# Kernel optimization log

Hardware: AMD Instinct MI355X
Metric: run time of the kernel (lower is better)

Reference implementation:

```python
import jax, jax.numpy as jnp
import numpy as np

ALPHA = 0.2
NEG_INF = -9e15


def setup_inputs() -> dict:
    key = jax.random.key(0)
    k1, k2, k3, k4 = jax.random.split(key, 4)
    B, N, C_IN, C_OUT, R, H = 8, 1024, 256, 256, 4, 4
    node_feats = jax.random.normal(k1, (B, N, C_IN), dtype=jnp.float32)
    adj_matrix = jax.random.randint(k2, (B, N, N, R), 0, 2, dtype=jnp.int32)
    # xavier_uniform with gain=1.414 for Linear(c_in, c_out) weights
    lim_w = 1.414 * np.sqrt(6.0 / (C_IN + C_OUT))
    W = jax.random.uniform(k3, (R, C_IN, C_OUT), minval=-lim_w, maxval=lim_w, dtype=jnp.float32)
    c_per = C_OUT // H
    lim_a = 1.414 * np.sqrt(6.0 / (H + 2 * c_per))
    a = jax.random.uniform(k4, (R, H, 2 * c_per), minval=-lim_a, maxval=lim_a, dtype=jnp.float32)
    return {"node_feats": node_feats, "adj_matrix": adj_matrix, "W": W, "a": a}


def reference(node_feats, adj_matrix, W, a):
    B, N, _ = node_feats.shape
    R, H = a.shape[0], a.shape[1]
    C = a.shape[2] // 2  # per-head feature dim
    out = jnp.zeros((B, N, H, C), dtype=node_feats.dtype)
    for r in range(R):
        # per-relation projection: [B,N,H,C]
        f = jnp.einsum('bnc,cd->bnd', node_feats, W[r]).reshape(B, N, H, C)
        a_l, a_r = a[r, :, :C], a[r, :, C:]
        # attention logit decomposes: a . [f_i || f_j] = a_l . f_i + a_r . f_j
        li = jnp.einsum('bnhc,hc->bnh', f, a_l)  # source-node term
        lj = jnp.einsum('bnhc,hc->bnh', f, a_r)  # target-node term
        logits = jax.nn.leaky_relu(li[:, :, None, :] + lj[:, None, :, :], ALPHA)  # [B,N,N,H]
        mask = adj_matrix[..., r] != 0  # [B,N,N]
        logits = jnp.where(mask[..., None], logits, NEG_INF)
        probs = jax.nn.softmax(logits, axis=2)
        out = out + jnp.einsum('bijh,bjhc->bihc', probs, f)
    # concat_heads=True
    return out.reshape(B, N, H * C)
```

## Files before the change

kernel.cpp:

```cpp
#include <hip/hip_runtime.h>
#include <math.h>

#define Bsz 8
#define Nn 1024
#define CIN 256
#define COUT 256
#define NR 4
#define NH 4

typedef unsigned short u16;
typedef __attribute__((ext_vector_type(8))) short bf16x8;
typedef __attribute__((ext_vector_type(4))) float f32x4;
typedef __attribute__((ext_vector_type(2))) float f32x2;

#define OFF_LIP (16u << 20)
#define OFF_LJP ((16u << 20) + (512u << 10))
#define OFF_ADJM (17u << 20)
#define OFF_XBF (21u << 20)
#define OFF_WFRAG (25u << 20)
#define OFF_WAL ((25u << 20) + (512u << 10))
#define OFF_WAR ((25u << 20) + (528u << 10))

#define LOG2E 1.4426950408889634f

__device__ __forceinline__ short f2bf(float x) {
  union { float f; unsigned u; } v; v.f = x;
  unsigned r = (v.u + 0x7FFFu + ((v.u >> 16) & 1u)) >> 16;
  return (short)r;
}

__device__ __forceinline__ float fast_exp2(float x) {
#if __has_builtin(__builtin_amdgcn_exp2f)
  return __builtin_amdgcn_exp2f(x);
#else
  return exp2f(x);
#endif
}

__device__ __forceinline__ int sbfe1(unsigned v, int bit) {
#if __has_builtin(__builtin_amdgcn_sbfe)
  return __builtin_amdgcn_sbfe((int)v, bit, 1);
#else
  return ((int)(v << (31 - bit))) >> 31;
#endif
}

__device__ __forceinline__ unsigned perm_hi16(unsigned hi, unsigned lo) {
#if __has_builtin(__builtin_amdgcn_perm)
  return __builtin_amdgcn_perm(hi, lo, 0x07060302u);
#else
  return (lo >> 16) | (hi & 0xFFFF0000u);
#endif
}

__global__ __launch_bounds__(256, 4)
void gatt_packprep(const int4* __restrict__ adj4, const float* __restrict__ W,
                   const float* __restrict__ a, unsigned long long* __restrict__ adjm,
                   u16* __restrict__ Wfrag, float* __restrict__ wa_l,
                   float* __restrict__ wa_r) {
  const int t = threadIdx.x;
  if (blockIdx.x < 32768) {
    const int wid = blockIdx.x * 4 + (t >> 6);
    const int lane = t & 63;
    const int jw = wid & 15;
    const int i = (wid >> 4) & 1023;
    const int b = wid >> 14;
    const int j = jw * 64 + lane;
    const int4 av = adj4[(size_t)(b * Nn + i) * Nn + j];
    const unsigned long long b0 = __ballot(av.x != 0);
    const unsigned long long b1 = __ballot(av.y != 0);
    const unsigned long long b2 = __ballot(av.z != 0);
    const unsigned long long b3 = __ballot(av.w != 0);
    if (lane < 4) {
      unsigned long long v = (lane == 0) ? b0 : (lane == 1) ? b1 : (lane == 2) ? b2 : b3;
      adjm[((size_t)((b * Nn + i) * NR + lane)) * 16 + jw] = v;
    }
  } else if (blockIdx.x < 32768 + 32) {
    const int bid2 = blockIdx.x - 32768;
    const int r = bid2 >> 3, kc = bid2 & 7;
    const int cg = t >> 4, mm = t & 15;
    float wv[32];
#pragma unroll 8
    for (int kk = 0; kk < 32; ++kk)
      wv[kk] = W[(size_t)r * 65536 + (size_t)(kc * 32 + kk) * COUT + t];
    u16* base = Wfrag + (size_t)r * 65536 + (size_t)(cg * 8 + kc) * 512 + mm * 8;
#pragma unroll
    for (int quad = 0; quad < 4; ++quad) {
      u16 pk[8];
#pragma unroll
      for (int e = 0; e < 8; ++e) pk[e] = (u16)f2bf(wv[quad * 8 + e]);
      *(int4*)(base + quad * 128) = *(int4*)pk;
    }
  } else {
    const int cb = blockIdx.x - 32768 - 32;
    const int r = cb >> 2, h = cb & 3;
    float sl = 0.f, sr = 0.f;
    const float* Wp = W + (size_t)r * 65536 + (size_t)t * COUT + h * 64;
    const float* ap = a + r * 512 + h * 128;
#pragma unroll 8
    for (int c = 0; c < 64; ++c) {
      const float wv = Wp[c];
      sl = fmaf(wv, ap[c], sl);
      sr = fmaf(wv, ap[64 + c], sr);
    }
    wa_l[(size_t)cb * CIN + t] = sl;
    wa_r[(size_t)cb * CIN + t] = sr;
  }
}

__global__ __launch_bounds__(256, 4)
void gatt_logitx(const float* __restrict__ X, const float4* __restrict__ wal4,
                 const float4* __restrict__ war4, float* __restrict__ Lip,
                 float* __restrict__ Ljp, u16* __restrict__ Xbf) {
  __shared__ float Xs[16 * 260];
  const int t = threadIdx.x;
  const int row0 = blockIdx.x * 16;
  {
    const int il = t >> 4, kq = t & 15;
    const float4* xp = (const float4*)(X + (size_t)(row0 + il) * CIN + kq * 16);
    float4 v[4];
    u16 pk[16];
#pragma unroll
    for (int u = 0; u < 4; ++u) {
      v[u] = xp[u];
      pk[u * 4 + 0] = (u16)f2bf(v[u].x);
      pk[u * 4 + 1] = (u16)f2bf(v[u].y);
      pk[u * 4 + 2] = (u16)f2bf(v[u].z);
      pk[u * 4 + 3] = (u16)f2bf(v[u].w);
    }
    float4* dst = (float4*)(Xs + il * 260 + kq * 16);
#pragma unroll
    for (int u = 0; u < 4; ++u) dst[u] = v[u];
    u16* xb = Xbf + (size_t)(row0 + il) * CIN + kq * 16;
    *(int4*)xb = *(int4*)pk;
    *(int4*)(xb + 8) = *(int4*)(pk + 8);
  }
  __syncthreads();
  const int rl = t >> 4, combo = t & 15;
  float li = 0.f, lj = 0.f;
#pragma unroll 8
  for (int k4 = 0; k4 < 64; ++k4) {
    const float4 x4 = *(const float4*)(Xs + rl * 260 + k4 * 4);
    const float4 wl = wal4[combo * 64 + k4];
    const float4 wr = war4[combo * 64 + k4];
    li += x4.x * wl.x + x4.y * wl.y + x4.z * wl.z + x4.w * wl.w;
    lj += x4.x * wr.x + x4.y * wr.y + x4.z * wr.z + x4.w * wr.w;
  }
  const int g = row0 + rl, b = g >> 10, n = g & 1023;
  const size_t idx = ((size_t)(combo * Bsz + b)) * Nn + n;
  Lip[idx] = li * LOG2E;
  Ljp[idx] = lj * LOG2E;
}

__global__ __launch_bounds__(256, 4)
void gatt_fgemm(const u16* __restrict__ Xbf, const u16* __restrict__ Wfrag,
                u16* __restrict__ fTf) {
  const int t = threadIdx.x;
  const int r = blockIdx.x & 3, b = (blockIdx.x >> 2) & 7, ntl = blockIdx.x >> 5;
  const int n0 = ntl * 32;
  const int lane = t & 63, w = t >> 6;
  const int m = lane & 15, quad = lane >> 4;

  const u16* wbase = Wfrag + (size_t)r * 65536 + (size_t)(w * 4) * 8 * 512 + lane * 8;
  const u16* xbase = Xbf + (size_t)(b * Nn + n0 + m) * CIN + quad * 8;

  f32x4 acc[4][2];
#pragma unroll
  for (int ct = 0; ct < 4; ++ct)
#pragma unroll
    for (int nt = 0; nt < 2; ++nt) acc[ct][nt] = (f32x4){0.f, 0.f, 0.f, 0.f};

#pragma unroll
  for (int kc = 0; kc < 8; ++kc) {
    bf16x8 af[4], bfr[2];
#pragma unroll
    for (int ct = 0; ct < 4; ++ct)
      af[ct] = *(const bf16x8*)(wbase + (size_t)(ct * 8 + kc) * 512);
#pragma unroll
    for (int nt = 0; nt < 2; ++nt)
      bfr[nt] = *(const bf16x8*)(xbase + (size_t)(nt * 16) * CIN + kc * 32);
#pragma unroll
    for (int ct = 0; ct < 4; ++ct)
#pragma unroll
      for (int nt = 0; nt < 2; ++nt)
        acc[ct][nt] = __builtin_amdgcn_mfma_f32_16x16x32_bf16(af[ct], bfr[nt], acc[ct][nt], 0, 0, 0);
  }

  u16* fragbase = fTf + (size_t)(((r * Bsz + b) * 4 + w) * 128) * 512;
  const int jb = n0 >> 5;
  const int e = m & 7;
#pragma unroll
  for (int ct = 0; ct < 4; ++ct) {
#pragma unroll
    for (int nt = 0; nt < 2; ++nt) {
      const int qt = nt * 2 + (m >> 3);
      u16* dst = fragbase + (size_t)((jb * 4 + ct) * 512) + (qt * 16 + quad * 4) * 8 + e;
#pragma unroll
      for (int p = 0; p < 4; ++p) dst[p * 8] = (u16)f2bf(acc[ct][nt][p]);
    }
  }
}

__global__ __launch_bounds__(256, 4)
void gatt_attn(const unsigned long long* __restrict__ adjm,
               const u16* __restrict__ fTf, const float* __restrict__ Lip,
               const float* __restrict__ Ljp, float* __restrict__ out) {
  const int t = threadIdx.x;
  const int b = blockIdx.x & 7;
  const int i0 = (blockIdx.x >> 3) * 16;
  const int h = t >> 6, lane = t & 63;
  const int m = lane & 15, quad = lane >> 4;
  const int qo = quad * 8;

  bf16x8 ones;
#pragma unroll
  for (int e = 0; e < 8; ++e) ones[e] = (short)0x3F80;

  float outsum[4][4];
#pragma unroll
  for (int nt = 0; nt < 4; ++nt)
#pragma unroll
    for (int p = 0; p < 4; ++p) outsum[nt][p] = 0.f;

  for (int r = 0; r < NR; ++r) {
    const float liv = Lip[((size_t)((r * NH + h) * Bsz + b)) * Nn + i0 + m];
    const float* ljh = Ljp + ((size_t)((r * NH + h) * Bsz + b)) * Nn;
    const unsigned long long* amp = adjm + ((size_t)((b * Nn + i0 + m) * NR + r)) * 16;
    const bf16x8* fp = (const bf16x8*)fTf + (size_t)((r * Bsz + b) * 4 + h) * 8192;

    f32x4 acc[4], den;
    den = (f32x4){0.f, 0.f, 0.f, 0.f};
#pragma unroll
    for (int nt = 0; nt < 4; ++nt) acc[nt] = (f32x4){0.f, 0.f, 0.f, 0.f};

    for (int jq = 0; jq < 16; ++jq) {
      const uint2 mw = *(const uint2*)(amp + jq);
#pragma unroll
      for (int half = 0; half < 2; ++half) {
        const int jb = jq * 2 + half;
        const unsigned mb = (half ? mw.y : mw.x) >> qo;
        const f32x2* lj2p = (const f32x2*)(ljh + jb * 32 + qo);
        bf16x8 bfr[4];
#pragma unroll
        for (int nt = 0; nt < 4; ++nt) bfr[nt] = fp[(jb * 4 + nt) * 64 + lane];
        const f32x2 li2 = {liv, liv};
        unsigned afu[4];
#pragma unroll
        for (int pr = 0; pr < 4; ++pr) {
          const f32x2 s2 = li2 + lj2p[pr];
          const f32x2 s02 = s2 * 0.2f;
          const float t0 = fmaxf(s2.x, s02.x);
          const float t1 = fmaxf(s2.y, s02.y);
          const unsigned e0 =
              __float_as_uint(fast_exp2(t0)) & (unsigned)sbfe1(mb, 2 * pr);
          const unsigned e1 =
              __float_as_uint(fast_exp2(t1)) & (unsigned)sbfe1(mb, 2 * pr + 1);
          afu[pr] = perm_hi16(e1, e0);
        }
        union { unsigned u[4]; bf16x8 v; } af;
        af.u[0] = afu[0]; af.u[1] = afu[1]; af.u[2] = afu[2]; af.u[3] = afu[3];
        den = __builtin_amdgcn_mfma_f32_16x16x32_bf16(af.v, ones, den, 0, 0, 0);
#pragma unroll
        for (int nt = 0; nt < 4; ++nt)
          acc[nt] = __builtin_amdgcn_mfma_f32_16x16x32_bf16(af.v, bfr[nt], acc[nt], 0, 0, 0);
      }
    }

#pragma unroll
    for (int p = 0; p < 4; ++p) {
      const float inv = __builtin_amdgcn_rcpf(den[p]);
#pragma unroll
      for (int nt = 0; nt < 4; ++nt) outsum[nt][p] = fmaf(acc[nt][p], inv, outsum[nt][p]);
    }
  }

#pragma unroll
  for (int p = 0; p < 4; ++p) {
    const int i = i0 + quad * 4 + p;
    float* op = out + ((size_t)(b * Nn) + i) * COUT + h * 64 + m;
#pragma unroll
    for (int nt = 0; nt < 4; ++nt) op[nt * 16] = outsum[nt][p];
  }
}

extern "C" void kernel_launch(void* const* d_in, const int* in_sizes, int n_in,
                              void* d_out, int out_size, void* d_ws, size_t ws_size,
                              hipStream_t stream) {
  const float* X = (const float*)d_in[0];
  const int4* adj4 = (const int4*)d_in[1];
  const float* W = (const float*)d_in[2];
  const float* a = (const float*)d_in[3];
  float* out = (float*)d_out;

  char* ws = (char*)d_ws;
  u16* fTf = (u16*)ws;
  float* Lip = (float*)(ws + OFF_LIP);
  float* Ljp = (float*)(ws + OFF_LJP);
  unsigned long long* adjm = (unsigned long long*)(ws + OFF_ADJM);
  u16* Xbf = (u16*)(ws + OFF_XBF);
  u16* Wfrag = (u16*)(ws + OFF_WFRAG);
  float* wa_l = (float*)(ws + OFF_WAL);
  float* wa_r = (float*)(ws + OFF_WAR);

  gatt_packprep<<<dim3(32816), dim3(256), 0, stream>>>(adj4, W, a, adjm, Wfrag,
                                                       wa_l, wa_r);
  gatt_logitx<<<dim3(512), dim3(256), 0, stream>>>(X, (const float4*)wa_l,
                                                   (const float4*)wa_r, Lip, Ljp, Xbf);
  gatt_fgemm<<<dim3(1024), dim3(256), 0, stream>>>(Xbf, Wfrag, fTf);
  gatt_attn<<<dim3(512), dim3(256), 0, stream>>>(adjm, fTf, Lip, Ljp, out);
}
```

Before: 322.0 us.

## Split relations across waves and reuse F fragments over two row tiles

The attention kernel now gives each wave one (relation, head) pair instead of looping over all four relations serially, and each wave processes 32 query rows (two 16-row tiles) so every loaded F fragment feeds twice as many MFMAs. Per-relation normalized results are staged in shared memory and summed across relations after a barrier, then written with vectorized stores. This exposes more parallelism per block and halves global fragment traffic per output. In exchange it adds about 70KB of LDS and a block-wide sync, and doubles accumulator registers, which may limit occupancy.

```diff
diff --git a/kernel.cpp b/kernel.cpp
--- a/kernel.cpp
+++ b/kernel.cpp
@@ -201,48 +201,58 @@
   }
 }
 
-__global__ __launch_bounds__(256, 4)
+__global__ __launch_bounds__(512, 4)
 void gatt_attn(const unsigned long long* __restrict__ adjm,
                const u16* __restrict__ fTf, const float* __restrict__ Lip,
                const float* __restrict__ Ljp, float* __restrict__ out) {
+  __shared__ float lred[8 * 2184];
+
   const int t = threadIdx.x;
   const int b = blockIdx.x & 7;
-  const int i0 = (blockIdx.x >> 3) * 16;
-  const int h = t >> 6, lane = t & 63;
+  const int hpair = (blockIdx.x >> 3) & 1;
+  const int i0 = (blockIdx.x >> 4) * 32;
+  const int w = t >> 6, lane = t & 63;
+  const int hl = w & 1, r = w >> 1;
+  const int h = hpair * 2 + hl;
   const int m = lane & 15, quad = lane >> 4;
   const int qo = quad * 8;
 
+  const float* lipb = Lip + ((size_t)((r * NH + h) * Bsz + b)) * Nn;
+  const float li0 = lipb[i0 + m];
+  const float li1 = lipb[i0 + 16 + m];
+  const float* ljh = Ljp + ((size_t)((r * NH + h) * Bsz + b)) * Nn;
+  const unsigned long long* amp0 = adjm + ((size_t)((b * Nn + i0 + m) * NR + r)) * 16;
+  const unsigned long long* amp1 = amp0 + (size_t)16 * NR * 16;
+  const bf16x8* fp = (const bf16x8*)fTf + (size_t)((r * Bsz + b) * 4 + h) * 8192;
+
   bf16x8 ones;
 #pragma unroll
   for (int e = 0; e < 8; ++e) ones[e] = (short)0x3F80;
 
-  float outsum[4][4];
-#pragma unroll
-  for (int nt = 0; nt < 4; ++nt)
-#pragma unroll
-    for (int p = 0; p < 4; ++p) outsum[nt][p] = 0.f;
-
-  for (int r = 0; r < NR; ++r) {
-    const float liv = Lip[((size_t)((r * NH + h) * Bsz + b)) * Nn + i0 + m];
-    const float* ljh = Ljp + ((size_t)((r * NH + h) * Bsz + b)) * Nn;
-    const unsigned long long* amp = adjm + ((size_t)((b * Nn + i0 + m) * NR + r)) * 16;
-    const bf16x8* fp = (const bf16x8*)fTf + (size_t)((r * Bsz + b) * 4 + h) * 8192;
-
-    f32x4 acc[4], den;
-    den = (f32x4){0.f, 0.f, 0.f, 0.f};
-#pragma unroll
-    for (int nt = 0; nt < 4; ++nt) acc[nt] = (f32x4){0.f, 0.f, 0.f, 0.f};
-
-    for (int jq = 0; jq < 16; ++jq) {
-      const uint2 mw = *(const uint2*)(amp + jq);
-#pragma unroll
-      for (int half = 0; half < 2; ++half) {
-        const int jb = jq * 2 + half;
-        const unsigned mb = (half ? mw.y : mw.x) >> qo;
-        const f32x2* lj2p = (const f32x2*)(ljh + jb * 32 + qo);
-        bf16x8 bfr[4];
-#pragma unroll
-        for (int nt = 0; nt < 4; ++nt) bfr[nt] = fp[(jb * 4 + nt) * 64 + lane];
+  f32x4 acc[2][4], den[2];
+#pragma unroll
+  for (int iw = 0; iw < 2; ++iw) {
+    den[iw] = (f32x4){0.f, 0.f, 0.f, 0.f};
+#pragma unroll
+    for (int nt = 0; nt < 4; ++nt) acc[iw][nt] = (f32x4){0.f, 0.f, 0.f, 0.f};
+  }
+
+  for (int jq = 0; jq < 16; ++jq) {
+    const uint2 mw0 = *(const uint2*)(amp0 + jq);
+    const uint2 mw1 = *(const uint2*)(amp1 + jq);
+#pragma unroll
+    for (int half = 0; half < 2; ++half) {
+      const int jb = jq * 2 + half;
+      const unsigned w0 = half ? mw0.y : mw0.x;
+      const unsigned w1 = half ? mw1.y : mw1.x;
+      const f32x2* lj2p = (const f32x2*)(ljh + jb * 32 + qo);
+      bf16x8 bfr[4];
+#pragma unroll
+      for (int nt = 0; nt < 4; ++nt) bfr[nt] = fp[(jb * 4 + nt) * 64 + lane];
+#pragma unroll
+      for (int iw = 0; iw < 2; ++iw) {
+        const float liv = iw ? li1 : li0;
+        const unsigned mb = (iw ? w1 : w0) >> qo;
         const f32x2 li2 = {liv, liv};
         unsigned afu[4];
 #pragma unroll
@@ -259,27 +269,45 @@
         }
         union { unsigned u[4]; bf16x8 v; } af;
         af.u[0] = afu[0]; af.u[1] = afu[1]; af.u[2] = afu[2]; af.u[3] = afu[3];
-        den = __builtin_amdgcn_mfma_f32_16x16x32_bf16(af.v, ones, den, 0, 0, 0);
+        den[iw] = __builtin_amdgcn_mfma_f32_16x16x32_bf16(af.v, ones, den[iw], 0, 0, 0);
 #pragma unroll
         for (int nt = 0; nt < 4; ++nt)
-          acc[nt] = __builtin_amdgcn_mfma_f32_16x16x32_bf16(af.v, bfr[nt], acc[nt], 0, 0, 0);
+          acc[iw][nt] = __builtin_amdgcn_mfma_f32_16x16x32_bf16(af.v, bfr[nt], acc[iw][nt], 0, 0, 0);
       }
     }
-
+  }
+
+  float* ltile = lred + (hl * 4 + r) * 2184;
+#pragma unroll
+  for (int iw = 0; iw < 2; ++iw) {
 #pragma unroll
     for (int p = 0; p < 4; ++p) {
-      const float inv = __builtin_amdgcn_rcpf(den[p]);
-#pragma unroll
-      for (int nt = 0; nt < 4; ++nt) outsum[nt][p] = fmaf(acc[nt][p], inv, outsum[nt][p]);
-    }
-  }
-
-#pragma unroll
-  for (int p = 0; p < 4; ++p) {
-    const int i = i0 + quad * 4 + p;
-    float* op = out + ((size_t)(b * Nn) + i) * COUT + h * 64 + m;
-#pragma unroll
-    for (int nt = 0; nt < 4; ++nt) op[nt * 16] = outsum[nt][p];
+      const float inv = __builtin_amdgcn_rcpf(den[iw][p]);
+      float* lp = ltile + (iw * 16 + quad * 4 + p) * 68 + m;
+#pragma unroll
+      for (int nt = 0; nt < 4; ++nt) lp[nt * 16] = acc[iw][nt][p] * inv;
+    }
+  }
+  __syncthreads();
+
+  {
+    const int ci = t >> 4;
+    const int cc = (t & 15) * 8;
+    const int chl = cc >> 6;
+    const int cin = cc & 63;
+    const float* basep = lred + chl * 4 * 2184 + ci * 68 + cin;
+    f32x4 s0 = (f32x4){0.f, 0.f, 0.f, 0.f};
+    f32x4 s1 = (f32x4){0.f, 0.f, 0.f, 0.f};
+#pragma unroll
+    for (int rr = 0; rr < 4; ++rr) {
+      const f32x4 a0 = *(const f32x4*)(basep + rr * 2184);
+      const f32x4 a1 = *(const f32x4*)(basep + rr * 2184 + 4);
+      s0 += a0;
+      s1 += a1;
+    }
+    float* op = out + ((size_t)(b * Nn) + i0 + ci) * COUT + hpair * 128 + cc;
+    *(f32x4*)op = s0;
+    *(f32x4*)(op + 4) = s1;
   }
 }
 
@@ -307,5 +335,5 @@
   gatt_logitx<<<dim3(512), dim3(256), 0, stream>>>(X, (const float4*)wa_l,
                                                    (const float4*)wa_r, Lip, Ljp, Xbf);
   gatt_fgemm<<<dim3(1024), dim3(256), 0, stream>>>(Xbf, Wfrag, fTf);
-  gatt_attn<<<dim3(512), dim3(256), 0, stream>>>(adjm, fTf, Lip, Ljp, out);
-}
+  gatt_attn<<<dim3(512), dim3(512), 0, stream>>>(adjm, fTf, Lip, Ljp, out);
+}
```

Result: faster. 296.1 us (-8.0%).
